# Kernel tuning notes

Hardware: AMD Instinct MI355X
Metric: run time of the kernel (lower is better)

## Reference

```python
import jax, jax.numpy as jnp
import numpy as np

N = 20000       # nodes
E = 320000      # edges (before self-loops)
F_IN = 128
HID = 128
HEADS = 4
OUT_DIM = 2
B = 64          # graphs in batch
SLOPE = 0.2     # GATv2 leaky_relu negative slope (PyG default)


def _glorot(key, shape):
    fan_in, fan_out = shape[0], shape[1]
    limit = np.sqrt(6.0 / (fan_in + fan_out)).astype(np.float32)
    return jax.random.uniform(key, shape, jnp.float32, -limit, limit)


def setup_inputs() -> dict:
    key = jax.random.key(0)
    ks = jax.random.split(key, 24)
    inp = {
        'x': jax.random.normal(ks[0], (N, F_IN), jnp.float32),
        'edge_src': jax.random.randint(ks[1], (E,), 0, N),
        'edge_dst': jax.random.randint(ks[2], (E,), 0, N),
        'batch': jnp.sort(jax.random.randint(ks[3], (N,), 0, B)),
        # layer 1: in=F_IN, out=HEADS*HID, concat
        'Wl1': _glorot(ks[4], (F_IN, HEADS * HID)),
        'Wr1': _glorot(ks[5], (F_IN, HEADS * HID)),
        'bl1': jnp.zeros((HEADS * HID,), jnp.float32),
        'br1': jnp.zeros((HEADS * HID,), jnp.float32),
        'att1': _glorot(ks[6], (HEADS, HID)),
        'bias1': jnp.zeros((HEADS * HID,), jnp.float32),
        # layer 2: in=HEADS*HID, out=HEADS*HID, concat
        'Wl2': _glorot(ks[7], (HEADS * HID, HEADS * HID)),
        'Wr2': _glorot(ks[8], (HEADS * HID, HEADS * HID)),
        'bl2': jnp.zeros((HEADS * HID,), jnp.float32),
        'br2': jnp.zeros((HEADS * HID,), jnp.float32),
        'att2': _glorot(ks[9], (HEADS, HID)),
        'bias2': jnp.zeros((HEADS * HID,), jnp.float32),
        # layer 3: in=HEADS*HID, heads=1, concat=False -> out=HID
        'Wl3': _glorot(ks[10], (HEADS * HID, HID)),
        'Wr3': _glorot(ks[11], (HEADS * HID, HID)),
        'bl3': jnp.zeros((HID,), jnp.float32),
        'br3': jnp.zeros((HID,), jnp.float32),
        'att3': _glorot(ks[12], (1, HID)),
        'bias3': jnp.zeros((HID,), jnp.float32),
        # output MLP
        'W_mlp1': _glorot(ks[13], (HID, HID)),
        'b_mlp1': jnp.zeros((HID,), jnp.float32),
        'W_mlp2': _glorot(ks[14], (HID, OUT_DIM)),
        'b_mlp2': jnp.zeros((OUT_DIM,), jnp.float32),
    }
    return inp


def gatv2_layer(x, src, dst, Wl, Wr, bl, br, att, bias, concat):
    """PyG GATv2Conv (eval mode): alpha_ij = softmax_j over N(i) of a^T LeakyReLU(xl_j + xr_i)."""
    H, C = att.shape
    n = x.shape[0]
    xl = (x @ Wl + bl).reshape(n, H, C)   # source transform
    e = jax.nn.leaky_relu(xl[src] + (x @ Wr + br).reshape(n, H, C)[dst], SLOPE)  # [E,H,C]
    logits = jnp.einsum('ehc,hc->eh', e, att)                                    # [E,H]
    # segment softmax over destination node
    m = jax.ops.segment_max(logits, dst, num_segments=n)
    alpha = jnp.exp(logits - m[dst])
    denom = jax.ops.segment_sum(alpha, dst, num_segments=n)
    alpha = alpha / denom[dst]
    out = jax.ops.segment_sum(xl[src] * alpha[..., None], dst, num_segments=n)   # [N,H,C]
    out = out.reshape(n, H * C) if concat else out.mean(axis=1)
    return out + bias


def reference(x, edge_src, edge_dst, batch,
              Wl1, Wr1, bl1, br1, att1, bias1,
              Wl2, Wr2, bl2, br2, att2, bias2,
              Wl3, Wr3, bl3, br3, att3, bias3,
              W_mlp1, b_mlp1, W_mlp2, b_mlp2):
    n = x.shape[0]
    loop = jnp.arange(n, dtype=edge_src.dtype)
    src = jnp.concatenate([edge_src, loop])   # PyG add_self_loops=True
    dst = jnp.concatenate([edge_dst, loop])

    h = jax.nn.elu(gatv2_layer(x, src, dst, Wl1, Wr1, bl1, br1, att1, bias1, True))
    h = jax.nn.elu(gatv2_layer(h, src, dst, Wl2, Wr2, bl2, br2, att2, bias2, True))
    h = jax.nn.elu(gatv2_layer(h, src, dst, Wl3, Wr3, bl3, br3, att3, bias3, False))

    # global_mean_pool over graph ids
    counts = jnp.maximum(jax.ops.segment_sum(jnp.ones((n,), h.dtype), batch, num_segments=B), 1.0)
    pooled = jax.ops.segment_sum(h, batch, num_segments=B) / counts[:, None]

    hidden = jax.nn.relu(pooled @ W_mlp1 + b_mlp1)
    return hidden @ W_mlp2 + b_mlp2
```

## Files before the change

### kernel.cpp

```cpp
#include <hip/hip_runtime.h>
#include <math.h>


typedef __attribute__((ext_vector_type(4))) float f32x4;
typedef __attribute__((ext_vector_type(8))) _Float16 f16x8;
typedef __attribute__((ext_vector_type(4))) _Float16 f16x4;
typedef __attribute__((ext_vector_type(2))) _Float16 f16x2;

__device__ __forceinline__ float elu1(float x) {
    return (x > 0.f) ? x : (__expf(x) - 1.f);
}
__device__ __forceinline__ f16x2 pk_leaky(f16x2 s) {
    const f16x2 slope = {(_Float16)0.2f, (_Float16)0.2f};
    return __builtin_elementwise_max(s, s * slope);
}

__global__ void zero32_kernel(int* __restrict__ p, int n) {
    int i = blockIdx.x * 256 + threadIdx.x;
    if (i < n) p[i] = 0;
}

__global__ void count_kernel(const int* __restrict__ dst, int* __restrict__ cnt,
                             int E, int N) {
    int e = blockIdx.x * 256 + threadIdx.x;
    if (e < E + N) {
        int d = (e < E) ? dst[e] : (e - E);
        atomicAdd(&cnt[d], 1);
    }
}

__global__ __launch_bounds__(256) void scan1_kernel(const int* __restrict__ cnt,
                                                    int* __restrict__ psum, int N) {
    __shared__ int red[256];
    int idx = blockIdx.x * 256 + threadIdx.x;
    red[threadIdx.x] = (idx < N) ? cnt[idx] : 0;
    __syncthreads();
    for (int s = 128; s > 0; s >>= 1) {
        if (threadIdx.x < s) red[threadIdx.x] += red[threadIdx.x + s];
        __syncthreads();
    }
    if (threadIdx.x == 0) psum[blockIdx.x] = red[0];
}
__global__ void scan2_kernel(int* __restrict__ psum, int nch) {
    if (threadIdx.x == 0) {
        int run = 0;
        for (int i = 0; i < nch; ++i) { int v = psum[i]; psum[i] = run; run += v; }
    }
}
__global__ __launch_bounds__(256) void scan3_kernel(const int* __restrict__ cnt,
                                                    const int* __restrict__ psum,
                                                    int* __restrict__ rowstart,
                                                    int* __restrict__ cursor, int N) {
    __shared__ int buf[256];
    int idx = blockIdx.x * 256 + threadIdx.x;
    int v = (idx < N) ? cnt[idx] : 0;
    buf[threadIdx.x] = v;
    __syncthreads();
    for (int off = 1; off < 256; off <<= 1) {
        int t = (threadIdx.x >= off) ? buf[threadIdx.x - off] : 0;
        __syncthreads();
        buf[threadIdx.x] += t;
        __syncthreads();
    }
    int excl = buf[threadIdx.x] - v + psum[blockIdx.x];
    if (idx < N) {
        rowstart[idx] = excl;
        cursor[idx]   = excl;
        if (idx == N - 1) rowstart[N] = excl + v;
    }
}

__global__ void scatter_kernel(const int* __restrict__ src, const int* __restrict__ dst,
                               int* __restrict__ cursor, int* __restrict__ csr_src,
                               int E, int N) {
    int e = blockIdx.x * 256 + threadIdx.x;
    if (e < E + N) {
        int d, s;
        if (e < E) { d = dst[e]; s = src[e]; }
        else       { d = e - E; s = e - E; }
        int pos = atomicAdd(&cursor[d], 1);
        csr_src[pos] = s;
    }
}

__global__ void boundary_kernel(const int* __restrict__ batch,
                                int* __restrict__ gstart, int N, int B) {
    int n = blockIdx.x * 256 + threadIdx.x;
    if (n > N) return;
    int cur  = (n < N) ? batch[n] : B;
    int prev = (n == 0) ? -1 : batch[n - 1];
    for (int g = prev + 1; g <= cur; ++g) gstart[g] = n;
}

__global__ void convA_kernel(const float* __restrict__ X, _Float16* __restrict__ A,
                             int n_valid, int n_total) {
    int i = (blockIdx.x * 256 + threadIdx.x) * 4;
    if (i >= n_total) return;
    float4 v = (i < n_valid) ? *(const float4*)(X + i) : make_float4(0.f, 0.f, 0.f, 0.f);
    f16x4 h;
    h.x = (_Float16)v.x; h.y = (_Float16)v.y;
    h.z = (_Float16)v.z; h.w = (_Float16)v.w;
    *(f16x4*)(A + i) = h;
}

__global__ __launch_bounds__(256) void convWT_kernel(
    const float* __restrict__ Wl, const float* __restrict__ Wr,
    _Float16* __restrict__ Bth, _Float16* __restrict__ Btl, int K, int Nh) {
    __shared__ float tile[32][33];
    int kb = blockIdx.x * 32;
    int nb = blockIdx.y * 32;
    int tx = threadIdx.x;
    int ty = threadIdx.y;
#pragma unroll
    for (int j = 0; j < 4; ++j) {
        int kk = kb + ty + j * 8;
        int nn = nb + tx;
        float v = (nn < Nh) ? Wl[(size_t)kk * Nh + nn]
                            : Wr[(size_t)kk * Nh + (nn - Nh)];
        tile[ty + j * 8][tx] = v;
    }
    __syncthreads();
#pragma unroll
    for (int j = 0; j < 4; ++j) {
        int nn = nb + ty + j * 8;
        int kk = kb + tx;
        float v = tile[tx][ty + j * 8];
        _Float16 h = (_Float16)v;
        Bth[(size_t)nn * K + kk] = h;
        Btl[(size_t)nn * K + kk] = (_Float16)(v - (float)h);
    }
}

#define SCW 132
__global__ __launch_bounds__(256, 1) void gemm_f16_kernel(
    const _Float16* __restrict__ A,
    const _Float16* __restrict__ Bh, const _Float16* __restrict__ Bl,
    const float* __restrict__ biasL, const float* __restrict__ biasR, int Nh_,
    _Float16* __restrict__ P, _Float16* __restrict__ Q, int K, int NT) {
    __shared__ __align__(16) char smem[49152];
    float* sC = (float*)(smem);

    const int tid  = threadIdx.x;
    const int lane = tid & 63;
    const int wv   = tid >> 6;
    const int wm   = wv & 1;
    const int wn   = wv >> 1;
    const int fm   = lane & 15;
    const int q    = lane >> 4;

    const int bi = blockIdx.x;
    const int kx = bi & 7;
    const int tt = bi >> 3;
    const int m0 = ((tt / NT) * 8 + kx) * 128;
    const int n0 = (tt % NT) * 128;

    const int r0  = lane >> 2;
    const int kco = (lane & 3) << 3;

    f32x4 acc[4][4];
#pragma unroll
    for (int i = 0; i < 4; ++i)
#pragma unroll
        for (int j = 0; j < 4; ++j) {
            acc[i][j].x = 0.f; acc[i][j].y = 0.f;
            acc[i][j].z = 0.f; acc[i][j].w = 0.f;
        }

    const int nIters = K >> 5;
    int cur = 0;
    {
        char* base = smem;
#pragma unroll
        for (int j = 0; j < 2; ++j) {
            int wc  = wv * 2 + j;
            int row = wc * 16 + r0;
            size_t ga = (size_t)(m0 + row) * K + kco;
            size_t gb = (size_t)(n0 + row) * K + kco;
            int lofs = wc * 1024;
            __builtin_amdgcn_global_load_lds(
                (const __attribute__((address_space(1))) void*)(A + ga),
                (__attribute__((address_space(3))) void*)(base + lofs), 16, 0, 0);
            __builtin_amdgcn_global_load_lds(
                (const __attribute__((address_space(1))) void*)(Bh + gb),
                (__attribute__((address_space(3))) void*)(base + 8192 + lofs), 16, 0, 0);
            __builtin_amdgcn_global_load_lds(
                (const __attribute__((address_space(1))) void*)(Bl + gb),
                (__attribute__((address_space(3))) void*)(base + 16384 + lofs), 16, 0, 0);
        }
    }
    for (int it = 0; it < nIters; ++it) {
        __syncthreads();
        if (it + 1 < nIters) {
            char* base = smem + (cur ^ 1) * 24576;
            int ks = (it + 1) << 5;
#pragma unroll
            for (int j = 0; j < 2; ++j) {
                int wc  = wv * 2 + j;
                int row = wc * 16 + r0;
                size_t ga = (size_t)(m0 + row) * K + ks + kco;
                size_t gb = (size_t)(n0 + row) * K + ks + kco;
                int lofs = wc * 1024;
                __builtin_amdgcn_global_load_lds(
                    (const __attribute__((address_space(1))) void*)(A + ga),
                    (__attribute__((address_space(3))) void*)(base + lofs), 16, 0, 0);
                __builtin_amdgcn_global_load_lds(
                    (const __attribute__((address_space(1))) void*)(Bh + gb),
                    (__attribute__((address_space(3))) void*)(base + 8192 + lofs), 16, 0, 0);
                __builtin_amdgcn_global_load_lds(
                    (const __attribute__((address_space(1))) void*)(Bl + gb),
                    (__attribute__((address_space(3))) void*)(base + 16384 + lofs), 16, 0, 0);
            }
        }

        _Float16* cA  = (_Float16*)(smem + cur * 24576);
        _Float16* cBh = (_Float16*)(smem + cur * 24576 + 8192);
        _Float16* cBl = (_Float16*)(smem + cur * 24576 + 16384);
        f16x8 ah[4];
#pragma unroll
        for (int mi = 0; mi < 4; ++mi)
            ah[mi] = *(const f16x8*)&cA[(wm * 64 + mi * 16 + fm) * 32 + q * 8];
#pragma unroll
        for (int ni = 0; ni < 4; ++ni) {
            int r = (wn * 64 + ni * 16 + fm) * 32 + q * 8;
            f16x8 bh = *(const f16x8*)&cBh[r];
            f16x8 bl = *(const f16x8*)&cBl[r];
#pragma unroll
            for (int mi = 0; mi < 4; ++mi) {
                acc[mi][ni] = __builtin_amdgcn_mfma_f32_16x16x32_f16(ah[mi], bh, acc[mi][ni], 0, 0, 0);
                acc[mi][ni] = __builtin_amdgcn_mfma_f32_16x16x32_f16(ah[mi], bl, acc[mi][ni], 0, 0, 0);
            }
        }
        cur ^= 1;
    }

    float bsv[4];
#pragma unroll
    for (int ni = 0; ni < 4; ++ni) {
        int col = n0 + wn * 64 + ni * 16 + fm;
        bsv[ni] = (col < Nh_) ? biasL[col] : biasR[col - Nh_];
    }

    _Float16* dstbase = (n0 < Nh_) ? P : Q;
    const int col0 = (n0 < Nh_) ? n0 : (n0 - Nh_);

#pragma unroll
    for (int c = 0; c < 2; ++c) {
        __syncthreads();
        if (wm == c) {
#pragma unroll
            for (int mi = 0; mi < 4; ++mi)
#pragma unroll
                for (int ni = 0; ni < 4; ++ni) {
                    int base = (mi * 16 + q * 4) * SCW + wn * 64 + ni * 16 + fm;
                    sC[base]           = acc[mi][ni].x + bsv[ni];
                    sC[base + SCW]     = acc[mi][ni].y + bsv[ni];
                    sC[base + 2 * SCW] = acc[mi][ni].z + bsv[ni];
                    sC[base + 3 * SCW] = acc[mi][ni].w + bsv[ni];
                }
        }
        __syncthreads();
#pragma unroll
        for (int j = 0; j < 8; ++j) {
            int flat = j * 256 + tid;
            int row  = flat >> 5;
            int col  = (flat & 31) * 4;
            f32x4 v = *(const f32x4*)(sC + row * SCW + col);
            f16x4 hv;
            hv.x = (_Float16)v.x; hv.y = (_Float16)v.y;
            hv.z = (_Float16)v.z; hv.w = (_Float16)v.w;
            *(f16x4*)(dstbase + (size_t)(m0 + c * 64 + row) * Nh_ + col0 + col) = hv;
        }
    }
}

__global__ __launch_bounds__(256) void gat_edge4_kernel(
    const _Float16* __restrict__ P, const _Float16* __restrict__ Q,
    const float* __restrict__ att, const float* __restrict__ bias,
    const int* __restrict__ rowstart, const int* __restrict__ srcs,
    _Float16* __restrict__ H, int N) {
    int wv = threadIdx.x >> 6;
    int lane = threadIdx.x & 63;
    int n = blockIdx.x * 4 + wv;
    if (n >= N) return;
    int c0 = lane * 8;

    f16x8 rv = *(const f16x8*)(Q + (size_t)n * 512 + c0);
    f16x2 r2[4], t2[4];
#pragma unroll
    for (int k = 0; k < 4; ++k) {
        r2[k].x = rv[2 * k]; r2[k].y = rv[2 * k + 1];
        t2[k].x = (_Float16)att[c0 + 2 * k];
        t2[k].y = (_Float16)att[c0 + 2 * k + 1];
    }

    float acc[8];
#pragma unroll
    for (int j = 0; j < 8; ++j) acc[j] = 0.f;
    float l_run = 0.f;

    int beg = rowstart[n], end = rowstart[n + 1];
    int i = beg;
    for (; i + 1 < end; i += 2) {
        int s0 = srcs[i];
        int s1 = srcs[i + 1];
        f16x8 hv0 = *(const f16x8*)(P + (size_t)s0 * 512 + c0);
        f16x8 hv1 = *(const f16x8*)(P + (size_t)s1 * 512 + c0);
        float p0 = 0.f, p1 = 0.f;
#pragma unroll
        for (int k = 0; k < 4; ++k) {
            f16x2 a0; a0.x = hv0[2 * k]; a0.y = hv0[2 * k + 1];
            f16x2 a1; a1.x = hv1[2 * k]; a1.y = hv1[2 * k + 1];
            p0 = __builtin_amdgcn_fdot2(pk_leaky(a0 + r2[k]), t2[k], p0, false);
            p1 = __builtin_amdgcn_fdot2(pk_leaky(a1 + r2[k]), t2[k], p1, false);
        }
        p0 += __shfl_xor(p0, 1, 16);
        p1 += __shfl_xor(p1, 1, 16);
        p0 += __shfl_xor(p0, 2, 16);
        p1 += __shfl_xor(p1, 2, 16);
        p0 += __shfl_xor(p0, 4, 16);
        p1 += __shfl_xor(p1, 4, 16);
        p0 += __shfl_xor(p0, 8, 16);
        p1 += __shfl_xor(p1, 8, 16);
        float w0 = __expf(p0);
        float w1 = __expf(p1);
        l_run += w0 + w1;
#pragma unroll
        for (int j = 0; j < 8; ++j) {
            float a = fmaf((float)hv0[j], w0, acc[j]);
            acc[j] = fmaf((float)hv1[j], w1, a);
        }
    }
    if (i < end) {
        int s = srcs[i];
        f16x8 hv = *(const f16x8*)(P + (size_t)s * 512 + c0);
        float p = 0.f;
#pragma unroll
        for (int k = 0; k < 4; ++k) {
            f16x2 a; a.x = hv[2 * k]; a.y = hv[2 * k + 1];
            p = __builtin_amdgcn_fdot2(pk_leaky(a + r2[k]), t2[k], p, false);
        }
        p += __shfl_xor(p, 1, 16);
        p += __shfl_xor(p, 2, 16);
        p += __shfl_xor(p, 4, 16);
        p += __shfl_xor(p, 8, 16);
        float w = __expf(p);
        l_run += w;
#pragma unroll
        for (int j = 0; j < 8; ++j)
            acc[j] = fmaf((float)hv[j], w, acc[j]);
    }
    float inv = 1.f / l_run;
    f16x8 oh;
#pragma unroll
    for (int j = 0; j < 8; ++j)
        oh[j] = (_Float16)elu1(acc[j] * inv + bias[c0 + j]);
    *(f16x8*)(H + (size_t)n * 512 + c0) = oh;
}

__global__ __launch_bounds__(256) void gat_edge1_kernel(
    const _Float16* __restrict__ P, const _Float16* __restrict__ Q,
    const float* __restrict__ att, const float* __restrict__ bias,
    const int* __restrict__ rowstart, const int* __restrict__ srcs,
    float* __restrict__ out, int N) {
    int wv = threadIdx.x >> 6;
    int lane = threadIdx.x & 63;
    int n = blockIdx.x * 4 + wv;
    if (n >= N) return;
    int c0 = lane * 2;

    f16x2 rv = *(const f16x2*)(Q + (size_t)n * 128 + c0);
    f16x2 t2;
    t2.x = (_Float16)att[c0];
    t2.y = (_Float16)att[c0 + 1];

    float acc0 = 0.f, acc1 = 0.f;
    float l_run = 0.f;

    int beg = rowstart[n], end = rowstart[n + 1];
    int i = beg;
    for (; i + 1 < end; i += 2) {
        int s0 = srcs[i];
        int s1 = srcs[i + 1];
        f16x2 h0 = *(const f16x2*)(P + (size_t)s0 * 128 + c0);
        f16x2 h1 = *(const f16x2*)(P + (size_t)s1 * 128 + c0);
        float p0 = __builtin_amdgcn_fdot2(pk_leaky(h0 + rv), t2, 0.f, false);
        float p1 = __builtin_amdgcn_fdot2(pk_leaky(h1 + rv), t2, 0.f, false);
        p0 += __shfl_xor(p0, 1, 64);
        p1 += __shfl_xor(p1, 1, 64);
        p0 += __shfl_xor(p0, 2, 64);
        p1 += __shfl_xor(p1, 2, 64);
        p0 += __shfl_xor(p0, 4, 64);
        p1 += __shfl_xor(p1, 4, 64);
        p0 += __shfl_xor(p0, 8, 64);
        p1 += __shfl_xor(p1, 8, 64);
        p0 += __shfl_xor(p0, 16, 64);
        p1 += __shfl_xor(p1, 16, 64);
        p0 += __shfl_xor(p0, 32, 64);
        p1 += __shfl_xor(p1, 32, 64);
        float w0 = __expf(p0);
        float w1 = __expf(p1);
        l_run += w0 + w1;
        acc0 = fmaf((float)h1.x, w1, fmaf((float)h0.x, w0, acc0));
        acc1 = fmaf((float)h1.y, w1, fmaf((float)h0.y, w0, acc1));
    }
    if (i < end) {
        int s = srcs[i];
        f16x2 hv = *(const f16x2*)(P + (size_t)s * 128 + c0);
        float p = __builtin_amdgcn_fdot2(pk_leaky(hv + rv), t2, 0.f, false);
        p += __shfl_xor(p, 1, 64);
        p += __shfl_xor(p, 2, 64);
        p += __shfl_xor(p, 4, 64);
        p += __shfl_xor(p, 8, 64);
        p += __shfl_xor(p, 16, 64);
        p += __shfl_xor(p, 32, 64);
        float w = __expf(p);
        l_run += w;
        acc0 = fmaf((float)hv.x, w, acc0);
        acc1 = fmaf((float)hv.y, w, acc1);
    }
    float inv = 1.f / l_run;
    float2 w2;
    w2.x = elu1(acc0 * inv + bias[c0]);
    w2.y = elu1(acc1 * inv + bias[c0 + 1]);
    *(float2*)(out + (size_t)n * 128 + c0) = w2;
}

__global__ __launch_bounds__(256) void pool2_kernel(
    const float* __restrict__ h3, const int* __restrict__ gstart,
    float* __restrict__ pooled) {
    __shared__ float red[256];
    int g = blockIdx.x;
    int c = threadIdx.x & 127;
    int h = threadIdx.x >> 7;
    int gs = gstart[g], ge = gstart[g + 1];
    float s = 0.f;
    for (int n = gs + h; n < ge; n += 2) s += h3[(size_t)n * 128 + c];
    red[threadIdx.x] = s;
    __syncthreads();
    if (h == 0) {
        float tot = red[c] + red[c + 128];
        float cnt = fmaxf((float)(ge - gs), 1.f);
        pooled[g * 128 + c] = tot / cnt;
    }
}

__global__ __launch_bounds__(128) void mlp_kernel(
    const float* __restrict__ pooled,
    const float* __restrict__ W1, const float* __restrict__ b1,
    const float* __restrict__ W2, const float* __restrict__ b2,
    float* __restrict__ out) {
    __shared__ float pr[128];
    __shared__ float2 red[128];
    int g = blockIdx.x;
    int t = threadIdx.x;
    pr[t] = pooled[g * 128 + t];
    __syncthreads();
    float h = b1[t];
#pragma unroll 4
    for (int k = 0; k < 128; ++k) h = fmaf(pr[k], W1[k * 128 + t], h);
    h = fmaxf(h, 0.0f);
    red[t] = make_float2(h * W2[t * 2], h * W2[t * 2 + 1]);
    __syncthreads();
    for (int s = 64; s > 0; s >>= 1) {
        if (t < s) {
            red[t].x += red[t + s].x;
            red[t].y += red[t + s].y;
        }
        __syncthreads();
    }
    if (t == 0) {
        out[g * 2]     = red[0].x + b2[0];
        out[g * 2 + 1] = red[0].y + b2[1];
    }
}

extern "C" void kernel_launch(void* const* d_in, const int* in_sizes, int n_in,
                              void* d_out, int out_size, void* d_ws, size_t ws_size,
                              hipStream_t stream) {
    const float* x     = (const float*)d_in[0];
    const int*   esrc  = (const int*)d_in[1];
    const int*   edst  = (const int*)d_in[2];
    const int*   batch = (const int*)d_in[3];
    const float* Wl1   = (const float*)d_in[4];
    const float* Wr1   = (const float*)d_in[5];
    const float* bl1   = (const float*)d_in[6];
    const float* br1   = (const float*)d_in[7];
    const float* att1  = (const float*)d_in[8];
    const float* bias1 = (const float*)d_in[9];
    const float* Wl2   = (const float*)d_in[10];
    const float* Wr2   = (const float*)d_in[11];
    const float* bl2   = (const float*)d_in[12];
    const float* br2   = (const float*)d_in[13];
    const float* att2  = (const float*)d_in[14];
    const float* bias2 = (const float*)d_in[15];
    const float* Wl3   = (const float*)d_in[16];
    const float* Wr3   = (const float*)d_in[17];
    const float* bl3   = (const float*)d_in[18];
    const float* br3   = (const float*)d_in[19];
    const float* att3  = (const float*)d_in[20];
    const float* bias3 = (const float*)d_in[21];
    const float* Wm1   = (const float*)d_in[22];
    const float* bm1   = (const float*)d_in[23];
    const float* Wm2   = (const float*)d_in[24];
    const float* bm2   = (const float*)d_in[25];

    int N  = in_sizes[0] / 128;
    int E  = in_sizes[1];
    int ET = E + N;
    int B  = out_size / 2;
    const int Mp = 160 * 128;
    int nch = (N + 255) / 256;

    char* ws = (char*)d_ws;
    size_t off = 0;
    auto alloc = [&](size_t bytes) -> void* {
        void* p = ws + off;
        off += (bytes + 255) & ~(size_t)255;
        return p;
    };
    _Float16* P    = (_Float16*)alloc((size_t)Mp * 512 * 2);
    _Float16* Q    = (_Float16*)alloc((size_t)Mp * 512 * 2);
    _Float16* A1   = (_Float16*)alloc((size_t)Mp * 128 * 2);
    _Float16* Hb   = (_Float16*)alloc((size_t)Mp * 512 * 2);
    _Float16* Wth1 = (_Float16*)alloc((size_t)1024 * 128 * 2);
    _Float16* Wtl1 = (_Float16*)alloc((size_t)1024 * 128 * 2);
    _Float16* Wth2 = (_Float16*)alloc((size_t)1024 * 512 * 2);
    _Float16* Wtl2 = (_Float16*)alloc((size_t)1024 * 512 * 2);
    _Float16* Wth3 = (_Float16*)alloc((size_t)256 * 512 * 2);
    _Float16* Wtl3 = (_Float16*)alloc((size_t)256 * 512 * 2);
    float*    R3   = (float*)alloc((size_t)Mp * 128 * 4);
    int*    cnt      = (int*)alloc((size_t)N * 4);
    int*    psum     = (int*)alloc((size_t)(nch + 1) * 4);
    int*    rowstart = (int*)alloc((size_t)(N + 1) * 4);
    int*    cursor   = (int*)alloc((size_t)N * 4);
    int*    csr_src  = (int*)alloc((size_t)ET * 4);
    int*    gstart   = (int*)alloc((size_t)(B + 1) * 4);
    float*  pooled   = (float*)alloc((size_t)B * 128 * 4);
    (void)ws_size;

    zero32_kernel<<<(N + 255) / 256, 256, 0, stream>>>(cnt, N);

    count_kernel<<<(ET + 255) / 256, 256, 0, stream>>>(edst, cnt, E, N);
    scan1_kernel<<<nch, 256, 0, stream>>>(cnt, psum, N);
    scan2_kernel<<<1, 64, 0, stream>>>(psum, nch);
    scan3_kernel<<<nch, 256, 0, stream>>>(cnt, psum, rowstart, cursor, N);
    scatter_kernel<<<(ET + 255) / 256, 256, 0, stream>>>(esrc, edst, cursor, csr_src, E, N);
    boundary_kernel<<<(N + 256) / 256, 256, 0, stream>>>(batch, gstart, N, B);

    convWT_kernel<<<dim3(4, 32),  dim3(32, 8), 0, stream>>>(Wl1, Wr1, Wth1, Wtl1, 128, 512);
    convWT_kernel<<<dim3(16, 32), dim3(32, 8), 0, stream>>>(Wl2, Wr2, Wth2, Wtl2, 512, 512);
    convWT_kernel<<<dim3(16, 8),  dim3(32, 8), 0, stream>>>(Wl3, Wr3, Wth3, Wtl3, 512, 128);

    convA_kernel<<<((Mp * 128 / 4) + 255) / 256, 256, 0, stream>>>(x, A1, N * 128, Mp * 128);

    int eblocks = (N + 3) / 4;

    gemm_f16_kernel<<<160 * 8, 256, 0, stream>>>(A1, Wth1, Wtl1, bl1, br1, 512, P, Q, 128, 8);
    gat_edge4_kernel<<<eblocks, 256, 0, stream>>>(P, Q, att1, bias1, rowstart, csr_src, Hb, N);

    gemm_f16_kernel<<<160 * 8, 256, 0, stream>>>(Hb, Wth2, Wtl2, bl2, br2, 512, P, Q, 512, 8);
    gat_edge4_kernel<<<eblocks, 256, 0, stream>>>(P, Q, att2, bias2, rowstart, csr_src, Hb, N);

    gemm_f16_kernel<<<160 * 2, 256, 0, stream>>>(Hb, Wth3, Wtl3, bl3, br3, 128, P, Q, 512, 2);
    gat_edge1_kernel<<<eblocks, 256, 0, stream>>>(P, Q, att3, bias3, rowstart, csr_src, R3, N);

    pool2_kernel<<<B, 256, 0, stream>>>(R3, gstart, pooled);
    mlp_kernel<<<B, 128, 0, stream>>>(pooled, Wm1, bm1, Wm2, bm2, (float*)d_out);
}
```

Measured before the change: 428.5 us.

## Unroll multi-head edge loop by four and split single-head edges across quarter-waves

The multi-head GATv2 aggregation kernel now processes four neighbor edges per iteration, clamping indices and zeroing the weights of padded slots, so more gathers are in flight and the tail loop is gone. The single-head layer-3 kernel is restructured so each 16-lane quarter-wave handles a different edge with 8 channels per lane. Partial sums are combined across quarters with shuffles at the end. This targets latency-bound irregular gathers and the long 64-lane shuffle reduction, at the cost of extra registers, redundant clamped loads on tails, and a final cross-quarter reduction.

New measurement: 423.3 us. No clear change (-1.2%).

```diff
diff --git a/kernel.cpp b/kernel.cpp
--- a/kernel.cpp
+++ b/kernel.cpp
@@ -299,55 +299,49 @@
     float l_run = 0.f;
 
     int beg = rowstart[n], end = rowstart[n + 1];
-    int i = beg;
-    for (; i + 1 < end; i += 2) {
-        int s0 = srcs[i];
-        int s1 = srcs[i + 1];
-        f16x8 hv0 = *(const f16x8*)(P + (size_t)s0 * 512 + c0);
-        f16x8 hv1 = *(const f16x8*)(P + (size_t)s1 * 512 + c0);
-        float p0 = 0.f, p1 = 0.f;
+    int last = end - 1;
+    for (int base = beg; base < end; base += 4) {
+        int rem = end - base;
+        int e1 = base + 1, e2 = base + 2, e3 = base + 3;
+        int s0 = srcs[base];
+        int s1 = srcs[e1 < last ? e1 : last];
+        int s2 = srcs[e2 < last ? e2 : last];
+        int s3 = srcs[e3 < last ? e3 : last];
+        f16x8 h0 = *(const f16x8*)(P + (size_t)s0 * 512 + c0);
+        f16x8 h1 = *(const f16x8*)(P + (size_t)s1 * 512 + c0);
+        f16x8 h2 = *(const f16x8*)(P + (size_t)s2 * 512 + c0);
+        f16x8 h3 = *(const f16x8*)(P + (size_t)s3 * 512 + c0);
+        float p0 = 0.f, p1 = 0.f, p2 = 0.f, p3 = 0.f;
 #pragma unroll
         for (int k = 0; k < 4; ++k) {
-            f16x2 a0; a0.x = hv0[2 * k]; a0.y = hv0[2 * k + 1];
-            f16x2 a1; a1.x = hv1[2 * k]; a1.y = hv1[2 * k + 1];
+            f16x2 a0; a0.x = h0[2 * k]; a0.y = h0[2 * k + 1];
+            f16x2 a1; a1.x = h1[2 * k]; a1.y = h1[2 * k + 1];
+            f16x2 a2; a2.x = h2[2 * k]; a2.y = h2[2 * k + 1];
+            f16x2 a3; a3.x = h3[2 * k]; a3.y = h3[2 * k + 1];
             p0 = __builtin_amdgcn_fdot2(pk_leaky(a0 + r2[k]), t2[k], p0, false);
             p1 = __builtin_amdgcn_fdot2(pk_leaky(a1 + r2[k]), t2[k], p1, false);
-        }
-        p0 += __shfl_xor(p0, 1, 16);
-        p1 += __shfl_xor(p1, 1, 16);
-        p0 += __shfl_xor(p0, 2, 16);
-        p1 += __shfl_xor(p1, 2, 16);
-        p0 += __shfl_xor(p0, 4, 16);
-        p1 += __shfl_xor(p1, 4, 16);
-        p0 += __shfl_xor(p0, 8, 16);
-        p1 += __shfl_xor(p1, 8, 16);
+            p2 = __builtin_amdgcn_fdot2(pk_leaky(a2 + r2[k]), t2[k], p2, false);
+            p3 = __builtin_amdgcn_fdot2(pk_leaky(a3 + r2[k]), t2[k], p3, false);
+        }
+#pragma unroll
+        for (int m = 1; m < 16; m <<= 1) {
+            p0 += __shfl_xor(p0, m, 16);
+            p1 += __shfl_xor(p1, m, 16);
+            p2 += __shfl_xor(p2, m, 16);
+            p3 += __shfl_xor(p3, m, 16);
+        }
         float w0 = __expf(p0);
-        float w1 = __expf(p1);
-        l_run += w0 + w1;
+        float w1 = (rem > 1) ? __expf(p1) : 0.f;
+        float w2 = (rem > 2) ? __expf(p2) : 0.f;
+        float w3 = (rem > 3) ? __expf(p3) : 0.f;
+        l_run += (w0 + w1) + (w2 + w3);
 #pragma unroll
         for (int j = 0; j < 8; ++j) {
-            float a = fmaf((float)hv0[j], w0, acc[j]);
-            acc[j] = fmaf((float)hv1[j], w1, a);
-        }
-    }
-    if (i < end) {
-        int s = srcs[i];
-        f16x8 hv = *(const f16x8*)(P + (size_t)s * 512 + c0);
-        float p = 0.f;
-#pragma unroll
-        for (int k = 0; k < 4; ++k) {
-            f16x2 a; a.x = hv[2 * k]; a.y = hv[2 * k + 1];
-            p = __builtin_amdgcn_fdot2(pk_leaky(a + r2[k]), t2[k], p, false);
-        }
-        p += __shfl_xor(p, 1, 16);
-        p += __shfl_xor(p, 2, 16);
-        p += __shfl_xor(p, 4, 16);
-        p += __shfl_xor(p, 8, 16);
-        float w = __expf(p);
-        l_run += w;
-#pragma unroll
-        for (int j = 0; j < 8; ++j)
-            acc[j] = fmaf((float)hv[j], w, acc[j]);
+            float a = fmaf((float)h0[j], w0, acc[j]);
+            a = fmaf((float)h1[j], w1, a);
+            a = fmaf((float)h2[j], w2, a);
+            acc[j] = fmaf((float)h3[j], w3, a);
+        }
     }
     float inv = 1.f / l_run;
     f16x8 oh;
@@ -366,63 +360,57 @@
     int lane = threadIdx.x & 63;
     int n = blockIdx.x * 4 + wv;
     if (n >= N) return;
-    int c0 = lane * 2;
-
-    f16x2 rv = *(const f16x2*)(Q + (size_t)n * 128 + c0);
-    f16x2 t2;
-    t2.x = (_Float16)att[c0];
-    t2.y = (_Float16)att[c0 + 1];
-
-    float acc0 = 0.f, acc1 = 0.f;
+    int qd = lane >> 4;
+    int lq = lane & 15;
+    int c0 = lq * 8;
+
+    f16x8 rv = *(const f16x8*)(Q + (size_t)n * 128 + c0);
+    f16x2 r2[4], t2[4];
+#pragma unroll
+    for (int k = 0; k < 4; ++k) {
+        r2[k].x = rv[2 * k]; r2[k].y = rv[2 * k + 1];
+        t2[k].x = (_Float16)att[c0 + 2 * k];
+        t2[k].y = (_Float16)att[c0 + 2 * k + 1];
+    }
+
+    float acc[8];
+#pragma unroll
+    for (int j = 0; j < 8; ++j) acc[j] = 0.f;
     float l_run = 0.f;
 
     int beg = rowstart[n], end = rowstart[n + 1];
-    int i = beg;
-    for (; i + 1 < end; i += 2) {
-        int s0 = srcs[i];
-        int s1 = srcs[i + 1];
-        f16x2 h0 = *(const f16x2*)(P + (size_t)s0 * 128 + c0);
-        f16x2 h1 = *(const f16x2*)(P + (size_t)s1 * 128 + c0);
-        float p0 = __builtin_amdgcn_fdot2(pk_leaky(h0 + rv), t2, 0.f, false);
-        float p1 = __builtin_amdgcn_fdot2(pk_leaky(h1 + rv), t2, 0.f, false);
-        p0 += __shfl_xor(p0, 1, 64);
-        p1 += __shfl_xor(p1, 1, 64);
-        p0 += __shfl_xor(p0, 2, 64);
-        p1 += __shfl_xor(p1, 2, 64);
-        p0 += __shfl_xor(p0, 4, 64);
-        p1 += __shfl_xor(p1, 4, 64);
-        p0 += __shfl_xor(p0, 8, 64);
-        p1 += __shfl_xor(p1, 8, 64);
-        p0 += __shfl_xor(p0, 16, 64);
-        p1 += __shfl_xor(p1, 16, 64);
-        p0 += __shfl_xor(p0, 32, 64);
-        p1 += __shfl_xor(p1, 32, 64);
-        float w0 = __expf(p0);
-        float w1 = __expf(p1);
-        l_run += w0 + w1;
-        acc0 = fmaf((float)h1.x, w1, fmaf((float)h0.x, w0, acc0));
-        acc1 = fmaf((float)h1.y, w1, fmaf((float)h0.y, w0, acc1));
-    }
-    if (i < end) {
-        int s = srcs[i];
-        f16x2 hv = *(const f16x2*)(P + (size_t)s * 128 + c0);
-        float p = __builtin_amdgcn_fdot2(pk_leaky(hv + rv), t2, 0.f, false);
-        p += __shfl_xor(p, 1, 64);
-        p += __shfl_xor(p, 2, 64);
-        p += __shfl_xor(p, 4, 64);
-        p += __shfl_xor(p, 8, 64);
-        p += __shfl_xor(p, 16, 64);
-        p += __shfl_xor(p, 32, 64);
+    for (int e = beg + qd; e < end; e += 4) {
+        int s = srcs[e];
+        f16x8 hv = *(const f16x8*)(P + (size_t)s * 128 + c0);
+        float p = 0.f;
+#pragma unroll
+        for (int k = 0; k < 4; ++k) {
+            f16x2 a; a.x = hv[2 * k]; a.y = hv[2 * k + 1];
+            p = __builtin_amdgcn_fdot2(pk_leaky(a + r2[k]), t2[k], p, false);
+        }
+        p += __shfl_xor(p, 1, 16);
+        p += __shfl_xor(p, 2, 16);
+        p += __shfl_xor(p, 4, 16);
+        p += __shfl_xor(p, 8, 16);
         float w = __expf(p);
         l_run += w;
-        acc0 = fmaf((float)hv.x, w, acc0);
-        acc1 = fmaf((float)hv.y, w, acc1);
+#pragma unroll
+        for (int j = 0; j < 8; ++j)
+            acc[j] = fmaf((float)hv[j], w, acc[j]);
+    }
+    l_run += __shfl_xor(l_run, 16, 64);
+    l_run += __shfl_xor(l_run, 32, 64);
+#pragma unroll
+    for (int j = 0; j < 8; ++j) {
+        acc[j] += __shfl_xor(acc[j], 16, 64);
+        acc[j] += __shfl_xor(acc[j], 32, 64);
     }
     float inv = 1.f / l_run;
+    int cw = c0 + qd * 2;
     float2 w2;
-    w2.x = elu1(acc0 * inv + bias[c0]);
-    w2.y = elu1(acc1 * inv + bias[c0 + 1]);
-    *(float2*)(out + (size_t)n * 128 + c0) = w2;
+    w2.x = elu1(acc[qd * 2]     * inv + bias[cw]);
+    w2.y = elu1(acc[qd * 2 + 1] * inv + bias[cw + 1]);
+    *(float2*)(out + (size_t)n * 128 + cw) = w2;
 }
 
 __global__ __launch_bounds__(256) void pool2_kernel(
```
